# Optimization experiments

Measured on AMD Instinct MI355X. Metric: run time of the kernel, lower is better.

Reference implementation:

```python
import jax, jax.numpy as jnp
import numpy as np

B, N, DIM_IN, DIM_OUT, CHEB_K, EMBED_DIM = 64, 2048, 64, 64, 3, 10


def setup_inputs() -> dict:
    key = jax.random.key(0)
    k1, k2, k3, k4 = jax.random.split(key, 4)
    x = jax.random.normal(k1, (B, N, DIM_IN), dtype=jnp.float32)
    node_embeddings = jax.random.normal(k2, (N, EMBED_DIM), dtype=jnp.float32)
    # xavier-normal-like init for the pools
    w_std = (2.0 / (EMBED_DIM * CHEB_K * DIM_IN + DIM_OUT)) ** 0.5
    b_std = (2.0 / (EMBED_DIM + DIM_OUT)) ** 0.5
    weights_pool = jax.random.normal(k3, (EMBED_DIM, CHEB_K, DIM_IN, DIM_OUT), dtype=jnp.float32) * w_std
    bias_pool = jax.random.normal(k4, (EMBED_DIM, DIM_OUT), dtype=jnp.float32) * b_std
    return {"x": x, "node_embeddings": node_embeddings,
            "weights_pool": weights_pool, "bias_pool": bias_pool,
            "cheb_k": CHEB_K}


def reference(x, node_embeddings, weights_pool, bias_pool, cheb_k):
    n = node_embeddings.shape[0]
    # adaptive adjacency: softmax(relu(E E^T)) over neighbors
    supports = jax.nn.softmax(jax.nn.relu(node_embeddings @ node_embeddings.T), axis=1)
    # Chebyshev polynomial supports: T0 = I, T1 = A, Tk = 2 A T_{k-1} - T_{k-2}
    support_set = [jnp.eye(n, dtype=supports.dtype), supports]
    for _ in range(2, cheb_k):
        support_set.append(2.0 * supports @ support_set[-1] - support_set[-2])
    supports_k = jnp.stack(support_set, axis=0)  # [K, N, N]
    # per-node weights and bias synthesized from node embeddings
    weights = jnp.einsum('nd,dkio->nkio', node_embeddings, weights_pool)  # [N, K, I, O]
    bias = node_embeddings @ bias_pool                                    # [N, O]
    # graph convolution
    x_g = jnp.einsum('knm,bmc->bnkc', supports_k, x)                      # [B, N, K, I]
    out = jnp.einsum('bnki,nkio->bno', x_g, weights) + bias               # [B, N, O]
    return out
```

## Files before the change

kernel.cpp:

```cpp
#include <hip/hip_runtime.h>

#define NN 2048
#define BB 64
#define CC 64
#define ED 10
#define KK 3
#define JJ (BB * CC)

typedef unsigned short ushort_t;
typedef __attribute__((ext_vector_type(8))) short short8;
typedef __attribute__((ext_vector_type(4))) float f32x4;

typedef const __attribute__((address_space(1))) unsigned* gptr_t;
typedef __attribute__((address_space(3))) unsigned* lptr_t;

static __device__ __forceinline__ ushort_t f2bf(float f) {
    union { float f; unsigned u; } x{f};
    unsigned r = x.u + 0x7FFF + ((x.u >> 16) & 1);
    return (ushort_t)(r >> 16);
}
static __device__ __forceinline__ float bf2f(ushort_t h) {
    union { unsigned u; float f; } x;
    x.u = ((unsigned)h) << 16;
    return x.f;
}

__global__ __launch_bounds__(256) void prep_kernel(const float* __restrict__ E,
                                                   const float* __restrict__ x,
                                                   const float* __restrict__ Wp,
                                                   ushort_t* __restrict__ Ab,
                                                   ushort_t* __restrict__ xT,
                                                   ushort_t* __restrict__ xN,
                                                   ushort_t* __restrict__ WpT) {
    const int bid = blockIdx.x;
    const int tid = threadIdx.x;

    __shared__ float tb[64][68];
    __shared__ float red[8];

    if (bid < NN) {
        const int n = bid;
        float en[ED];
#pragma unroll
        for (int d = 0; d < ED; ++d) en[d] = E[n * ED + d];

        float sv[NN / 256];
        float lmax = 0.0f;
#pragma unroll
        for (int j = 0; j < NN / 256; ++j) {
            const int m = tid + j * 256;
            const float* Em = E + m * ED;
            float dot = 0.0f;
#pragma unroll
            for (int d = 0; d < ED; ++d) dot += en[d] * Em[d];
            float s = fmaxf(dot, 0.0f);
            sv[j] = s;
            lmax = fmaxf(lmax, s);
        }
#pragma unroll
        for (int off = 32; off > 0; off >>= 1) lmax = fmaxf(lmax, __shfl_down(lmax, off, 64));
        if ((tid & 63) == 0) red[tid >> 6] = lmax;
        __syncthreads();
        const float bmax = fmaxf(fmaxf(red[0], red[1]), fmaxf(red[2], red[3]));

        float lsum = 0.0f;
#pragma unroll
        for (int j = 0; j < NN / 256; ++j) {
            sv[j] = __expf(sv[j] - bmax);
            lsum += sv[j];
        }
#pragma unroll
        for (int off = 32; off > 0; off >>= 1) lsum += __shfl_down(lsum, off, 64);
        if ((tid & 63) == 0) red[4 + (tid >> 6)] = lsum;
        __syncthreads();
        const float inv = 1.0f / (red[4] + red[5] + red[6] + red[7]);

#pragma unroll
        for (int j = 0; j < NN / 256; ++j) {
            Ab[(size_t)n * NN + tid + j * 256] = f2bf(sv[j] * inv);
        }
    } else if (bid < 2 * NN) {
        const int t = bid - NN;
        const int n0 = (t & 31) * 64;
        const int b = t >> 5;

#pragma unroll
        for (int l = 0; l < 4; ++l) {
            const int idx = tid + l * 256;
            const int nn = idx >> 4;
            const int c4 = (idx & 15) << 2;
            const float4 v = *(const float4*)(x + ((size_t)b * NN + n0 + nn) * CC + c4);
            tb[c4 + 0][nn] = v.x;
            tb[c4 + 1][nn] = v.y;
            tb[c4 + 2][nn] = v.z;
            tb[c4 + 3][nn] = v.w;
        }
        __syncthreads();

#pragma unroll
        for (int l = 0; l < 2; ++l) {
            const int idx = tid + l * 256;
            const int c = idx >> 3;
            const int ch = (idx & 7) << 3;
            ushort_t pack[8];
#pragma unroll
            for (int e = 0; e < 8; ++e) pack[e] = f2bf(tb[c][ch + e]);
            *(float4*)(xT + (size_t)(b * 64 + c) * NN + n0 + ch) = *(float4*)pack;
        }
#pragma unroll
        for (int l = 0; l < 2; ++l) {
            const int idx = tid + l * 256;
            const int nn = idx >> 3;
            const int cg = (idx & 7) << 3;
            ushort_t pack[8];
#pragma unroll
            for (int e = 0; e < 8; ++e) pack[e] = f2bf(tb[cg + e][nn]);
            *(float4*)(xN + (size_t)(n0 + nn) * JJ + b * 64 + cg) = *(float4*)pack;
        }
    } else {
        const int dk = bid - 2 * NN;
        const float* src = Wp + (size_t)dk * CC * CC;

#pragma unroll
        for (int l = 0; l < 4; ++l) {
            const int idx = tid + l * 256;
            const int i = idx >> 4;
            const int o4 = (idx & 15) << 2;
            const float4 v = *(const float4*)(src + i * CC + o4);
            tb[o4 + 0][i] = v.x;
            tb[o4 + 1][i] = v.y;
            tb[o4 + 2][i] = v.z;
            tb[o4 + 3][i] = v.w;
        }
        __syncthreads();

#pragma unroll
        for (int l = 0; l < 2; ++l) {
            const int idx = tid + l * 256;
            const int o = idx >> 3;
            const int ic = (idx & 7) << 3;
            ushort_t pack[8];
#pragma unroll
            for (int e = 0; e < 8; ++e) pack[e] = f2bf(tb[o][ic + e]);
            *(float4*)(WpT + (size_t)dk * CC * CC + o * CC + ic) = *(float4*)pack;
        }
    }
}

__global__ __launch_bounds__(256) void trans_kernel(const ushort_t* __restrict__ Ab,
                                                    ushort_t* __restrict__ At) {
    const int bx = blockIdx.x;
    const int by = blockIdx.y;
    const int tid = threadIdx.x;
    __shared__ ushort_t tb[64][72];

#pragma unroll
    for (int l = 0; l < 2; ++l) {
        const int idx = tid + l * 256;
        const int r = idx >> 3;
        const int c0 = (idx & 7) << 3;
        const float4 v = *(const float4*)(Ab + (size_t)(by * 64 + r) * NN + bx * 64 + c0);
        const ushort_t* p = (const ushort_t*)&v;
#pragma unroll
        for (int e = 0; e < 8; ++e) tb[c0 + e][r] = p[e];
    }
    __syncthreads();
#pragma unroll
    for (int l = 0; l < 2; ++l) {
        const int idx = tid + l * 256;
        const int m = idx >> 3;
        const int c0 = (idx & 7) << 3;
        ushort_t pack[8];
#pragma unroll
        for (int e = 0; e < 8; ++e) pack[e] = tb[m][c0 + e];
        *(float4*)(At + (size_t)(bx * 64 + m) * NN + by * 64 + c0) = *(float4*)pack;
    }
}

__global__ __launch_bounds__(256) void gemm_t2(const ushort_t* __restrict__ A,
                                               const ushort_t* __restrict__ Bt,
                                               ushort_t* __restrict__ C) {
    const int j0 = blockIdx.x * 128;
    const int m0 = blockIdx.y * 128;
    const int tid = threadIdx.x;
    const int lane = tid & 63;
    const int l16 = lane & 15;
    const int quad = lane >> 4;
    const int w = tid >> 6;
    const int wm = (w >> 1) * 64;
    const int wj = (w & 1) * 64;
    const int lr = lane >> 3;
    const int lc = lane & 7;
    const int swz = lc ^ lr;

    __shared__ ushort_t As[2][128 * 64];
    __shared__ ushort_t Bs[2][128 * 64];

    f32x4 acc[4][4];
#pragma unroll
    for (int mi = 0; mi < 4; ++mi)
#pragma unroll
        for (int ji = 0; ji < 4; ++ji) acc[mi][ji] = (f32x4){0.f, 0.f, 0.f, 0.f};

#pragma unroll
    for (int inst = 0; inst < 4; ++inst) {
        const int rbase = w * 32 + inst * 8;
        const int row = rbase + lr;
        __builtin_amdgcn_global_load_lds(
            (gptr_t)(A + (size_t)(m0 + row) * NN + swz * 8),
            (lptr_t)&As[0][rbase * 64], 16, 0, 0);
        __builtin_amdgcn_global_load_lds(
            (gptr_t)(Bt + (size_t)(j0 + row) * NN + swz * 8),
            (lptr_t)&Bs[0][rbase * 64], 16, 0, 0);
    }

    for (int it = 0; it < NN / 64; ++it) {
        const int cur = it & 1;
        __syncthreads();

        if (it + 1 < NN / 64) {
            const int k0 = (it + 1) * 64;
#pragma unroll
            for (int inst = 0; inst < 4; ++inst) {
                const int rbase = w * 32 + inst * 8;
                const int row = rbase + lr;
                __builtin_amdgcn_global_load_lds(
                    (gptr_t)(A + (size_t)(m0 + row) * NN + k0 + swz * 8),
                    (lptr_t)&As[1 - cur][rbase * 64], 16, 0, 0);
                __builtin_amdgcn_global_load_lds(
                    (gptr_t)(Bt + (size_t)(j0 + row) * NN + k0 + swz * 8),
                    (lptr_t)&Bs[1 - cur][rbase * 64], 16, 0, 0);
            }
        }

#pragma unroll
        for (int ks = 0; ks < 64; ks += 32) {
            const int qb = (ks >> 3) + quad;
            short8 av[4], bv[4];
#pragma unroll
            for (int mi = 0; mi < 4; ++mi) {
                const int rA = wm + mi * 16 + l16;
                av[mi] = *(const short8*)&As[cur][rA * 64 + ((qb ^ (rA & 7)) << 3)];
            }
#pragma unroll
            for (int ji = 0; ji < 4; ++ji) {
                const int rB = wj + ji * 16 + l16;
                bv[ji] = *(const short8*)&Bs[cur][rB * 64 + ((qb ^ (rB & 7)) << 3)];
            }
#pragma unroll
            for (int mi = 0; mi < 4; ++mi)
#pragma unroll
                for (int ji = 0; ji < 4; ++ji)
                    acc[mi][ji] = __builtin_amdgcn_mfma_f32_16x16x32_bf16(
                        av[mi], bv[ji], acc[mi][ji], 0, 0, 0);
        }
    }

#pragma unroll
    for (int mi = 0; mi < 4; ++mi) {
#pragma unroll
        for (int ji = 0; ji < 4; ++ji) {
            const int j = j0 + wj + ji * 16 + l16;
            const int mb = m0 + wm + mi * 16 + quad * 4;
#pragma unroll
            for (int r = 0; r < 4; ++r) {
                const float v = 2.0f * acc[mi][ji][r] - ((mb + r) == j ? 1.0f : 0.0f);
                C[(size_t)(mb + r) * NN + j] = f2bf(v);
            }
        }
    }
}

#define STAGE_HALF(buf, h3, kt) do {                                                        \
    const ushort_t* s_ = ((h3) < 2) ? srcA : srcB;                                          \
    __builtin_amdgcn_global_load_lds(                                                       \
        (gptr_t)(s_ + (size_t)(((h3) & 1) * 2) * 64 * NN + (size_t)(kt) * 64),              \
        (lptr_t)&lds[buf][(h3) >= 2][(((h3) & 1) * 2) * 4096 + dstoff], 16, 0, 0);          \
    __builtin_amdgcn_global_load_lds(                                                       \
        (gptr_t)(s_ + (size_t)(((h3) & 1) * 2 + 1) * 64 * NN + (size_t)(kt) * 64),          \
        (lptr_t)&lds[buf][(h3) >= 2][(((h3) & 1) * 2 + 1) * 4096 + dstoff], 16, 0, 0);      \
} while (0)

#define LDA_Q(buf, qm) do {                                                                 \
    _Pragma("unroll") for (int mi_ = 0; mi_ < 4; ++mi_)                                     \
    _Pragma("unroll") for (int ks_ = 0; ks_ < 2; ++ks_)                                     \
        a[mi_][ks_] = *(const short8*)&lds[buf][0][((aRG + (qm) * 4 + mi_) * 2 + ks_) * 512 + rdofs]; \
} while (0)

#define LDB_Q(buf, qn) do {                                                                 \
    _Pragma("unroll") for (int ni_ = 0; ni_ < 2; ++ni_)                                     \
    _Pragma("unroll") for (int ks_ = 0; ks_ < 2; ++ks_)                                     \
        b[(qn) * 2 + ni_][ks_] = *(const short8*)&lds[buf][1][((bRG + (qn) * 2 + ni_) * 2 + ks_) * 512 + rdofs]; \
} while (0)

#define MFMA_Q(qm, qn) do {                                                                 \
    __builtin_amdgcn_s_setprio(1);                                                          \
    _Pragma("unroll") for (int mi_ = 0; mi_ < 4; ++mi_)                                     \
    _Pragma("unroll") for (int nn_ = 0; nn_ < 2; ++nn_) {                                   \
        acc[(qm) * 4 + mi_][(qn) * 2 + nn_] = __builtin_amdgcn_mfma_f32_16x16x32_bf16(      \
            a[mi_][0], b[(qn) * 2 + nn_][0], acc[(qm) * 4 + mi_][(qn) * 2 + nn_], 0, 0, 0); \
        acc[(qm) * 4 + mi_][(qn) * 2 + nn_] = __builtin_amdgcn_mfma_f32_16x16x32_bf16(      \
            a[mi_][1], b[(qn) * 2 + nn_][1], acc[(qm) * 4 + mi_][(qn) * 2 + nn_], 0, 0, 0); \
    }                                                                                       \
    __builtin_amdgcn_s_setprio(0);                                                          \
} while (0)

#define PH_SYNC do {                                                                        \
    __builtin_amdgcn_s_barrier();                                                           \
    asm volatile("s_waitcnt lgkmcnt(0)" ::: "memory");                                      \
    __builtin_amdgcn_sched_barrier(0);                                                      \
} while (0)

#define PH_END do {                                                                         \
    __builtin_amdgcn_sched_barrier(0);                                                      \
    __builtin_amdgcn_s_barrier();                                                           \
} while (0)

__global__ __launch_bounds__(512, 2) void gemm8(const ushort_t* __restrict__ Ab,
                                                const ushort_t* __restrict__ T2b,
                                                const ushort_t* __restrict__ Bt,
                                                ushort_t* __restrict__ y1N,
                                                ushort_t* __restrict__ y2N) {
    int bid = blockIdx.x;
    bid = (bid & 7) * 32 + (bid >> 3);
    const int bx = bid & 15;
    const int by = bid >> 4;
    const int j0 = bx * 256;
    const int m0 = by * 256;

    const ushort_t* Arows = (by < 8) ? (Ab + (size_t)m0 * NN) : (T2b + (size_t)(m0 - NN) * NN);
    const ushort_t* Brows = Bt + (size_t)j0 * NN;
    ushort_t* Crow = (by < 8) ? (y1N + (size_t)m0 * JJ) : (y2N + (size_t)(m0 - NN) * JJ);

    const int tid = threadIdx.x;
    const int w = tid >> 6;
    const int lane = tid & 63;
    const int l16 = lane & 15;
    const int quad = lane >> 4;
    const int wm = (w >> 2) * 128;
    const int wn = (w & 3) * 64;
    const int aRG = (w >> 2) * 8;
    const int bRG = (w & 3) * 4;
    const int rdofs = l16 * 32 + ((quad * 8) ^ ((l16 & 8) * 2));

    const int r16s = lane >> 2;
    const int cx = (lane & 3) ^ ((r16s >> 3) << 1);
    const int rowbase = (w >> 1) * 16 + r16s;
    const int kofs = (w & 1) * 32 + cx * 8;
    const ushort_t* srcA = Arows + (size_t)rowbase * NN + kofs;
    const ushort_t* srcB = Brows + (size_t)rowbase * NN + kofs;
    const int dstoff = tid * 8;

    __shared__ ushort_t lds[2][2][16384];

    f32x4 acc[8][4];
#pragma unroll
    for (int mi = 0; mi < 8; ++mi)
#pragma unroll
        for (int ni = 0; ni < 4; ++ni) acc[mi][ni] = (f32x4){0.f, 0.f, 0.f, 0.f};

    short8 a[4][2], b[4][2];

    STAGE_HALF(0, 0, 0); STAGE_HALF(0, 1, 0); STAGE_HALF(0, 2, 0); STAGE_HALF(0, 3, 0);
    STAGE_HALF(1, 0, 1); STAGE_HALF(1, 1, 1);
    asm volatile("s_waitcnt vmcnt(4)" ::: "memory");
    __builtin_amdgcn_s_barrier();

#pragma unroll 1
    for (int i = 0; i < 16; ++i) {
        const int tb_ = 2 * i + 1;
        const int ta2 = 2 * i + 2;
        const int tb2 = 2 * i + 3;
        const bool stg = (i < 15);

        LDA_Q(0, 0); LDB_Q(0, 0);
        STAGE_HALF(1, 2, tb_);
        PH_SYNC; MFMA_Q(0, 0); PH_END;
        LDB_Q(0, 1);
        STAGE_HALF(1, 3, tb_);
        PH_SYNC; MFMA_Q(0, 1); PH_END;
        LDA_Q(0, 1);
        if (stg) STAGE_HALF(0, 2, ta2);
        PH_SYNC; MFMA_Q(1, 1); PH_END;
        if (stg) { STAGE_HALF(0, 3, ta2); STAGE_HALF(0, 0, ta2); }
        __builtin_amdgcn_s_barrier();
        MFMA_Q(1, 0);
        __builtin_amdgcn_sched_barrier(0);
        if (stg) { asm volatile("s_waitcnt vmcnt(6)" ::: "memory"); }
        else     { asm volatile("s_waitcnt vmcnt(0)" ::: "memory"); }
        __builtin_amdgcn_s_barrier();

        LDA_Q(1, 0); LDB_Q(1, 0);
        if (stg) STAGE_HALF(0, 1, ta2);
        PH_SYNC; MFMA_Q(0, 0); PH_END;
        LDB_Q(1, 1);
        PH_SYNC; MFMA_Q(0, 1); PH_END;
        LDA_Q(1, 1);
        PH_SYNC; MFMA_Q(1, 1); PH_END;
        if (stg) { STAGE_HALF(1, 0, tb2); STAGE_HALF(1, 1, tb2); }
        __builtin_amdgcn_s_barrier();
        MFMA_Q(1, 0);
        __builtin_amdgcn_sched_barrier(0);
        if (stg) { asm volatile("s_waitcnt vmcnt(4)" ::: "memory"); }
        __builtin_amdgcn_s_barrier();
    }

#pragma unroll
    for (int mi = 0; mi < 8; ++mi) {
#pragma unroll
        for (int ni = 0; ni < 4; ++ni) {
            const int j = j0 + wn + ni * 16 + l16;
            const int mb = wm + mi * 16 + quad * 4;
#pragma unroll
            for (int r = 0; r < 4; ++r)
                Crow[(size_t)(mb + r) * JJ + j] = f2bf(acc[mi][ni][r]);
        }
    }
}

#undef STAGE_HALF
#undef LDA_Q
#undef LDB_Q
#undef MFMA_Q
#undef PH_SYNC
#undef PH_END

#define XLD 200
__global__ __launch_bounds__(256) void out_kernel(const float* __restrict__ E,
                                                  const ushort_t* __restrict__ WpT,
                                                  const float* __restrict__ bp,
                                                  const ushort_t* __restrict__ xN,
                                                  const ushort_t* __restrict__ y1N,
                                                  const ushort_t* __restrict__ y2N,
                                                  float* __restrict__ out) {
    const int n = blockIdx.x;
    const int tid = threadIdx.x;

    __shared__ ushort_t xg[BB * XLD];
    __shared__ ushort_t Wt[CC * XLD];
    __shared__ float en_s[ED];
    __shared__ float bias_s[CC];

    if (tid < ED) en_s[tid] = E[n * ED + tid];
    __syncthreads();

    float en[ED];
#pragma unroll
    for (int d = 0; d < ED; ++d) en[d] = en_s[d];

    if (tid < CC) {
        float bsum = 0.0f;
#pragma unroll
        for (int d = 0; d < ED; ++d) bsum += en[d] * bp[d * CC + tid];
        bias_s[tid] = bsum;
    }

#pragma unroll
    for (int k = 0; k < KK; ++k) {
        const ushort_t* src = (k == 0) ? xN : (k == 1) ? y1N : y2N;
        const float4* srow = (const float4*)(src + (size_t)n * JJ);
        for (int idx = tid; idx < JJ / 8; idx += 256) {
            *(float4*)&xg[(idx >> 3) * XLD + k * 64 + ((idx & 7) << 3)] = srow[idx];
        }
    }

    for (int t = tid; t < CC * 24; t += 256) {
        const int o = t / 24;
        const int kc = t % 24;
        const int k = kc >> 3;
        const int ic = (kc & 7) << 3;
        float s[8];
#pragma unroll
        for (int e = 0; e < 8; ++e) s[e] = 0.0f;
#pragma unroll
        for (int d = 0; d < ED; ++d) {
            const float4 wv4 = *(const float4*)(WpT + ((size_t)(d * KK + k) * CC + o) * CC + ic);
            const ushort_t* wp = (const ushort_t*)&wv4;
#pragma unroll
            for (int e = 0; e < 8; ++e) s[e] += en[d] * bf2f(wp[e]);
        }
        ushort_t pack[8];
#pragma unroll
        for (int e = 0; e < 8; ++e) pack[e] = f2bf(s[e]);
        *(float4*)&Wt[o * XLD + k * 64 + ic] = *(float4*)pack;
    }
    __syncthreads();

    const int lane = tid & 63;
    const int l16 = lane & 15;
    const int quad = lane >> 4;
    const int bm = (tid >> 6) * 16;

    f32x4 acc[4];
#pragma unroll
    for (int ji = 0; ji < 4; ++ji) acc[ji] = (f32x4){0.f, 0.f, 0.f, 0.f};

#pragma unroll
    for (int kc = 0; kc < 6; ++kc) {
        const short8 av = *(const short8*)&xg[(bm + l16) * XLD + kc * 32 + quad * 8];
#pragma unroll
        for (int ji = 0; ji < 4; ++ji) {
            const short8 bv = *(const short8*)&Wt[(ji * 16 + l16) * XLD + kc * 32 + quad * 8];
            acc[ji] = __builtin_amdgcn_mfma_f32_16x16x32_bf16(av, bv, acc[ji], 0, 0, 0);
        }
    }

#pragma unroll
    for (int ji = 0; ji < 4; ++ji) {
        const int o = ji * 16 + l16;
        const float bo = bias_s[o];
#pragma unroll
        for (int r = 0; r < 4; ++r) {
            const int b = bm + quad * 4 + r;
            out[((size_t)b * NN + n) * CC + o] = acc[ji][r] + bo;
        }
    }
}
#undef XLD

extern "C" void kernel_launch(void* const* d_in, const int* in_sizes, int n_in,
                              void* d_out, int out_size, void* d_ws, size_t ws_size,
                              hipStream_t stream) {
    const float* x  = (const float*)d_in[0];
    const float* E  = (const float*)d_in[1];
    const float* Wp = (const float*)d_in[2];
    const float* bp = (const float*)d_in[3];

    ushort_t* Ab  = (ushort_t*)d_ws;
    ushort_t* xT  = Ab + (size_t)NN * NN;
    ushort_t* xN  = xT + (size_t)JJ * NN;
    ushort_t* y1N = xN + (size_t)NN * JJ;
    ushort_t* y2N = y1N + (size_t)NN * JJ;
    ushort_t* At  = y2N;
    ushort_t* T2b = y2N + (size_t)NN * JJ;
    ushort_t* WpT = T2b + (size_t)NN * NN;
    float* out = (float*)d_out;

    prep_kernel<<<2 * NN + ED * KK, 256, 0, stream>>>(E, x, Wp, Ab, xT, xN, WpT);
    trans_kernel<<<dim3(32, 32), 256, 0, stream>>>(Ab, At);
    gemm_t2<<<dim3(16, 16), 256, 0, stream>>>(Ab, At, T2b);
    gemm8<<<256, 512, 0, stream>>>(Ab, T2b, xT, y1N, y2N);
    out_kernel<<<NN, 256, 0, stream>>>(E, WpT, bp, xN, y1N, y2N, out);
}
```

Measured before the change: 232.0 us.

## Overlap LDS fragment reads with MFMA and defer last quadrant across iterations

```diff
diff --git a/kernel.cpp b/kernel.cpp
--- a/kernel.cpp
+++ b/kernel.cpp
@@ -305,13 +305,13 @@
     __builtin_amdgcn_s_setprio(0);                                                          \
 } while (0)
 
-#define PH_SYNC do {                                                                        \
+#define WAIT_READS do {                                                                     \
     __builtin_amdgcn_s_barrier();                                                           \
     asm volatile("s_waitcnt lgkmcnt(0)" ::: "memory");                                      \
     __builtin_amdgcn_sched_barrier(0);                                                      \
 } while (0)
 
-#define PH_END do {                                                                         \
+#define REGION_END do {                                                                     \
     __builtin_amdgcn_sched_barrier(0);                                                      \
     __builtin_amdgcn_s_barrier();                                                           \
 } while (0)
@@ -373,37 +373,52 @@
         const int tb2 = 2 * i + 3;
         const bool stg = (i < 15);
 
+        if (i) MFMA_Q(1, 0);
         LDA_Q(0, 0); LDB_Q(0, 0);
         STAGE_HALF(1, 2, tb_);
-        PH_SYNC; MFMA_Q(0, 0); PH_END;
+        WAIT_READS;
+        MFMA_Q(0, 0);
         LDB_Q(0, 1);
+        REGION_END;
         STAGE_HALF(1, 3, tb_);
-        PH_SYNC; MFMA_Q(0, 1); PH_END;
+        WAIT_READS;
+        MFMA_Q(0, 1);
         LDA_Q(0, 1);
+        REGION_END;
         if (stg) STAGE_HALF(0, 2, ta2);
-        PH_SYNC; MFMA_Q(1, 1); PH_END;
-        if (stg) { STAGE_HALF(0, 3, ta2); STAGE_HALF(0, 0, ta2); }
+        WAIT_READS;
+        MFMA_Q(1, 1);
+        REGION_END;
+        if (stg) {
+            STAGE_HALF(0, 3, ta2); STAGE_HALF(0, 0, ta2);
+            asm volatile("s_waitcnt vmcnt(6)" ::: "memory");
+        } else {
+            asm volatile("s_waitcnt vmcnt(0)" ::: "memory");
+        }
         __builtin_amdgcn_s_barrier();
         MFMA_Q(1, 0);
-        __builtin_amdgcn_sched_barrier(0);
-        if (stg) { asm volatile("s_waitcnt vmcnt(6)" ::: "memory"); }
-        else     { asm volatile("s_waitcnt vmcnt(0)" ::: "memory"); }
-        __builtin_amdgcn_s_barrier();
-
         LDA_Q(1, 0); LDB_Q(1, 0);
         if (stg) STAGE_HALF(0, 1, ta2);
-        PH_SYNC; MFMA_Q(0, 0); PH_END;
+        WAIT_READS;
+        MFMA_Q(0, 0);
         LDB_Q(1, 1);
-        PH_SYNC; MFMA_Q(0, 1); PH_END;
+        REGION_END;
+        asm volatile("s_waitcnt lgkmcnt(0)" ::: "memory");
+        __builtin_amdgcn_sched_barrier(0);
+        MFMA_Q(0, 1);
         LDA_Q(1, 1);
-        PH_SYNC; MFMA_Q(1, 1); PH_END;
-        if (stg) { STAGE_HALF(1, 0, tb2); STAGE_HALF(1, 1, tb2); }
+        REGION_END;
+        asm volatile("s_waitcnt lgkmcnt(0)" ::: "memory");
+        __builtin_amdgcn_sched_barrier(0);
+        MFMA_Q(1, 1);
+        REGION_END;
+        if (stg) {
+            STAGE_HALF(1, 0, tb2); STAGE_HALF(1, 1, tb2);
+            asm volatile("s_waitcnt vmcnt(4)" ::: "memory");
+        }
         __builtin_amdgcn_s_barrier();
-        MFMA_Q(1, 0);
-        __builtin_amdgcn_sched_barrier(0);
-        if (stg) { asm volatile("s_waitcnt vmcnt(4)" ::: "memory"); }
-        __builtin_amdgcn_s_barrier();
-    }
+    }
+    MFMA_Q(1, 0);
 
 #pragma unroll
     for (int mi = 0; mi < 8; ++mi) {
@@ -422,8 +437,8 @@
 #undef LDA_Q
 #undef LDB_Q
 #undef MFMA_Q
-#undef PH_SYNC
-#undef PH_END
+#undef WAIT_READS
+#undef REGION_END
 
 #define XLD 200
 __global__ __launch_bounds__(256) void out_kernel(const float* __restrict__ E,
```

Measured after the change: 230.3 us. About the same (-0.7%).
